# Kernel tuning notes

Measured on AMD Instinct MI355X. Metric: run time of the kernel, lower is better.

The kernel has to match this reference:

```python
import jax, jax.numpy as jnp
import numpy as np

B, L, D, NHEAD, NLAYERS = 2, 2048, 256, 8, 8
NAMES = ['self', 'cross'] * 4


def setup_inputs() -> dict:
    key = jax.random.key(0)
    ks = jax.random.split(key, 6)
    w_scale = D ** -0.5  # keep activations well-scaled
    return {
        'f0': jax.random.normal(ks[0], (B, L, D), dtype=jnp.float32),
        'f1': jax.random.normal(ks[1], (B, L, D), dtype=jnp.float32),
        'Wq': jax.random.normal(ks[2], (NLAYERS, D, D), dtype=jnp.float32) * w_scale,
        'Wk': jax.random.normal(ks[3], (NLAYERS, D, D), dtype=jnp.float32) * w_scale,
        'Wv': jax.random.normal(ks[4], (NLAYERS, D, D), dtype=jnp.float32) * w_scale,
        'Wo': jax.random.normal(ks[5], (NLAYERS, D, D), dtype=jnp.float32) * w_scale,
    }


def _rope(x, inv_freq):
    # x: (B, L, D); RoPE over the FULL model dim (matches original, mixes heads)
    L_, D_ = x.shape[1], x.shape[2]
    t = jnp.arange(L_, dtype=jnp.float32)
    freqs = t[:, None] * inv_freq[None, :]          # (L, D/2)
    emb = jnp.concatenate([freqs, freqs], axis=-1)  # (L, D)
    x1, x2 = x[..., : D_ // 2], x[..., D_ // 2:]
    rot = jnp.concatenate([-x2, x1], axis=-1)
    return x * jnp.cos(emb) + rot * jnp.sin(emb)


def _attn(x, src, wq, wk, wv, wo, use_rope, inv_freq):
    b, l1, d = x.shape
    l2 = src.shape[1]
    dh = d // NHEAD
    q = x @ wq.T    # torch Linear: x @ W^T
    k = src @ wk.T
    v = src @ wv.T
    if use_rope:
        q = _rope(q, inv_freq)
        k = _rope(k, inv_freq)
    q = q.reshape(b, l1, NHEAD, dh)
    k = k.reshape(b, l2, NHEAD, dh)
    v = v.reshape(b, l2, NHEAD, dh)
    scores = jnp.einsum('bqhd,bkhd->bhqk', q, k) * (dh ** -0.5)
    out = jnp.einsum('bhqk,bkhd->bqhd', jax.nn.softmax(scores, axis=-1), v)
    return out.reshape(b, l1, d) @ wo.T


def reference(f0, f1, Wq, Wk, Wv, Wo):
    d = f0.shape[-1]
    inv_freq = 1.0 / (10000.0 ** (jnp.arange(0, d, 2, dtype=jnp.float32) / d))
    for i, name in enumerate(NAMES):
        if name == 'self':
            f0 = f0 + _attn(f0, f0, Wq[i], Wk[i], Wv[i], Wo[i], True, inv_freq)
            f1 = f1 + _attn(f1, f1, Wq[i], Wk[i], Wv[i], Wo[i], True, inv_freq)
        else:
            # sequential updates: second cross uses the UPDATED f0 (matches torch)
            f0 = f0 + _attn(f0, f1, Wq[i], Wk[i], Wv[i], Wo[i], False, inv_freq)
            f1 = f1 + _attn(f1, f0, Wq[i], Wk[i], Wv[i], Wo[i], False, inv_freq)
    return (f0, f1)
```

## Files before the change

### kernel.cpp

```cpp
#include <hip/hip_runtime.h>

#define BB   2
#define LL   2048
#define DD   256
#define NH   8
#define MM   (BB*LL)
#define NLAYERS 8
#define MMDD ((size_t)MM*DD)

typedef unsigned short ushort_t;
typedef __attribute__((ext_vector_type(8))) short  short8;
typedef __attribute__((ext_vector_type(4))) float  f32x4;
typedef __attribute__((ext_vector_type(4))) unsigned int u32x4;
typedef __attribute__((ext_vector_type(2))) unsigned int u32x2;

#define CSC 0.2550500394f

#define WAITV2 asm volatile("s_waitcnt vmcnt(2)" ::: "memory")
#define WAITV0 asm volatile("s_waitcnt vmcnt(0)" ::: "memory")
#define WAITLG asm volatile("s_waitcnt lgkmcnt(0)" ::: "memory")
#define BAR()  __builtin_amdgcn_s_barrier()
#define SCHED0 __builtin_amdgcn_sched_barrier(0)

__device__ __forceinline__ f32x4 mfma16(short8 a, short8 b, f32x4 c) {
    return __builtin_amdgcn_mfma_f32_16x16x32_bf16(a, b, c, 0, 0, 0);
}
__device__ __forceinline__ unsigned cvtpk(float lo, float hi) {
    unsigned r;
    asm volatile("v_cvt_pk_bf16_f32 %0, %1, %2" : "=v"(r) : "v"(lo), "v"(hi));
    return r;
}
__device__ __forceinline__ void pl32(unsigned &a, unsigned &b) {
    asm volatile("v_permlane32_swap_b32 %0, %1" : "+v"(a), "+v"(b));
}
__device__ __forceinline__ float bf2f(unsigned short h) {
    return __builtin_bit_cast(float, ((unsigned)h) << 16);
}
__device__ __forceinline__ void gll16(const void* gsrc, void* ldst) {
    __builtin_amdgcn_global_load_lds(
        (const __attribute__((address_space(1))) unsigned int*)gsrc,
        (__attribute__((address_space(3))) unsigned int*)ldst, 16, 0, 0);
}


__global__ __launch_bounds__(256) void initf(const float* __restrict__ f0,
                                             const float* __restrict__ f1,
                                             float* __restrict__ F,
                                             ushort_t* __restrict__ Fb) {
    int i = blockIdx.x * 256 + threadIdx.x;
    const float* src = (i < 131072) ? f0 : f1;
    int loc = i & 131071;
    const f32x4* p = (const f32x4*)(src + (size_t)loc * 8);
    f32x4 a = p[0], b = p[1];
    *(f32x4*)&F[(size_t)i * 8]     = a;
    *(f32x4*)&F[(size_t)i * 8 + 4] = b;
    u32x4 o = {cvtpk(a.x, a.y), cvtpk(a.z, a.w), cvtpk(b.x, b.y), cvtpk(b.z, b.w)};
    *(u32x4*)&Fb[(size_t)i * 8] = o;
}

__global__ __launch_bounds__(256) void wconv(const float* __restrict__ a,
                                             const float* __restrict__ b,
                                             const float* __restrict__ c,
                                             const float* __restrict__ d,
                                             ushort_t* __restrict__ out) {
    int i = blockIdx.x * 256 + threadIdx.x;
    int reg = i >> 16, loc = i & 65535;
    const float* src = reg == 0 ? a : reg == 1 ? b : reg == 2 ? c : d;
    const f32x4* p = (const f32x4*)(src + (size_t)loc * 8);
    f32x4 x = p[0], y = p[1];
    u32x4 o = {cvtpk(x.x, x.y), cvtpk(x.z, x.w), cvtpk(y.x, y.y), cvtpk(y.z, y.w)};
    *(u32x4*)&out[(size_t)reg * 524288 + (size_t)loc * 8] = o;
}

__global__ __launch_bounds__(128) void rtab(float* __restrict__ tab) {
    int p = blockIdx.x, j = threadIdx.x;
    float inv = __expf(-((float)j / 128.f) * 9.210340371976184f);
    float s, c;
    sincosf((float)p * inv, &s, &c);
    tab[(size_t)p * 256 + j]       = c;
    tab[(size_t)p * 256 + 128 + j] = s;
}

__global__ __launch_bounds__(256) void rope_qk(ushort_t* __restrict__ Qio,
                                               const ushort_t* __restrict__ KSrc,
                                               ushort_t* __restrict__ KT,
                                               const float* __restrict__ tab) {
    const bool isq = (blockIdx.y == 0);
    const ushort_t* S = isq ? Qio : KSrc;
    int t = threadIdx.x;
    int row = blockIdx.x * 8 + (t >> 5);
    int jj = (t & 31) * 4;
    int pos = row & (LL - 1);
    u32x2 va = *(const u32x2*)&S[(size_t)row * 256 + jj];
    u32x2 vb = *(const u32x2*)&S[(size_t)row * 256 + 128 + jj];
    f32x4 a = {bf2f(va.x & 0xffff), bf2f(va.x >> 16),
               bf2f(va.y & 0xffff), bf2f(va.y >> 16)};
    f32x4 b = {bf2f(vb.x & 0xffff), bf2f(vb.x >> 16),
               bf2f(vb.y & 0xffff), bf2f(vb.y >> 16)};
    f32x4 c = *(const f32x4*)&tab[(size_t)pos * 256 + jj];
    f32x4 s = *(const f32x4*)&tab[(size_t)pos * 256 + 128 + jj];
    f32x4 o1 = a * c - b * s;
    f32x4 o2 = b * c + a * s;
    if (isq) { o1 *= CSC; o2 *= CSC; }
    u32x2 p1 = {cvtpk(o1.x, o1.y), cvtpk(o1.z, o1.w)};
    u32x2 p2 = {cvtpk(o2.x, o2.y), cvtpk(o2.z, o2.w)};
    if (isq) {
        *(u32x2*)&Qio[(size_t)row * 256 + jj]       = p1;
        *(u32x2*)&Qio[(size_t)row * 256 + 128 + jj] = p2;
    } else {
        int z = row >> 11, key = row & 2047;
        int tt = key >> 6, kk = key & 63;
        int hA = jj >> 5, dh = jj & 31;
        int g = dh >> 3, e = dh & 7;
        size_t base = (size_t)tt * 2048 + (size_t)g * 512 + (size_t)kk * 8 + e;
        *(u32x2*)&KT[(size_t)(z * 8 + hA) * 65536 + base]     = p1;
        *(u32x2*)&KT[(size_t)(z * 8 + hA + 4) * 65536 + base] = p2;
    }
}

template<int NQ, int NK, int NV, int QMODE, int KMODE, int NTY>
__global__ __launch_bounds__(256) void gemm5(const ushort_t* __restrict__ X,
                                             const ushort_t* __restrict__ WQ,
                                             const ushort_t* __restrict__ WK,
                                             const ushort_t* __restrict__ WV,
                                             ushort_t* __restrict__ DQ,
                                             ushort_t* __restrict__ DK,
                                             ushort_t* __restrict__ DVT) {
    constexpr int NTX = NQ + NK + NV;
    __shared__ ushort_t Xb[3][4096];
    __shared__ ushort_t Wb[3][4096];
    const int tid = threadIdx.x, ln = tid & 63, w = tid >> 6;
    const int f = blockIdx.x;
    const int xcd = f & 7, s = f >> 3;
    const int bx = s % NTX, byg = s / NTX;
    const int by = xcd * (NTY / 8) + byg;
    const int m0 = by * 64;

    const ushort_t* W; ushort_t* DH; int n0, mode;
    if (NQ && bx < NQ)           { W = WQ; DH = DQ;  mode = QMODE; n0 = bx * 64; }
    else if (NK && bx < NQ + NK) { W = WK; DH = DK;  mode = KMODE; n0 = (bx - NQ) * 64; }
    else                         { W = WV; DH = DVT; mode = 3; n0 = (bx - NQ - NK) * 64; }

    auto stage = [&](int c, int buf) {
#pragma unroll
        for (int i = 0; i < 2; i++) {
            int sl = (w * 2 + i) * 64 + ln;
            int r = sl >> 3, x = sl & 7;
            int col = c * 64 + ((x ^ (r & 7)) << 3);
            gll16(X + (size_t)(m0 + r) * 256 + col, &Xb[buf][(w * 2 + i) * 512]);
            gll16(W + (size_t)(n0 + r) * 256 + col, &Wb[buf][(w * 2 + i) * 512]);
        }
    };

    const int ql = ln & 15, gq = ln >> 4;
    const int wm = w >> 1, wn = w & 1;
    f32x4 z4 = {0.f, 0.f, 0.f, 0.f};
    f32x4 acc[2][2] = {{z4, z4}, {z4, z4}};

    stage(0, 0);
    stage(1, 1);
#pragma unroll
    for (int c = 0; c < 4; c++) {
        if (c < 3) { asm volatile("s_waitcnt vmcnt(4)" ::: "memory"); } else { WAITV0; }
        BAR(); SCHED0;
        if (c + 2 < 4) stage(c + 2, (c + 2) % 3);
        const ushort_t* XL = Xb[c % 3];
        const ushort_t* WL = Wb[c % 3];
        __builtin_amdgcn_s_setprio(1);
#pragma unroll
        for (int ks = 0; ks < 2; ks++) {
            int cc = ks * 4 + gq;
            int r0 = 32 * wm + ql, r1 = r0 + 16;
            int nr0 = 32 * wn + ql, nr1 = nr0 + 16;
            short8 a0 = *(const short8*)&XL[(r0 * 8 + (cc ^ (r0 & 7))) * 8];
            short8 a1 = *(const short8*)&XL[(r1 * 8 + (cc ^ (r1 & 7))) * 8];
            short8 b0 = *(const short8*)&WL[(nr0 * 8 + (cc ^ (nr0 & 7))) * 8];
            short8 b1 = *(const short8*)&WL[(nr1 * 8 + (cc ^ (nr1 & 7))) * 8];
            acc[0][0] = mfma16(a0, b0, acc[0][0]);
            acc[0][1] = mfma16(a0, b1, acc[0][1]);
            acc[1][0] = mfma16(a1, b0, acc[1][0]);
            acc[1][1] = mfma16(a1, b1, acc[1][1]);
        }
        __builtin_amdgcn_s_setprio(0);
    }

    if (mode == 3) {
        float* scr = (float*)&Xb[0][0];
        __syncthreads();
#pragma unroll
        for (int mf = 0; mf < 2; mf++)
#pragma unroll
            for (int nf = 0; nf < 2; nf++)
#pragma unroll
                for (int r = 0; r < 4; r++) {
                    int nloc = 32 * wn + 16 * nf + ql;
                    int mloc = 32 * wm + 16 * mf + 4 * gq + r;
                    scr[nloc * 65 + mloc] = acc[mf][nf][r];
                }
        __syncthreads();
        int nloc = tid >> 2, mc = (tid & 3) * 16;
        int ng = n0 + nloc, hh = ng >> 5, dh = ng & 31;
        int mg = m0 + mc;
        int z = mg >> 11, key = mg & 2047;
        int tt = key >> 6;
        int ks = (mc >> 5) & 1, J = (mc >> 4) & 1;
        int cA = 4 * ks + 2 * J, cB = cA + 1;
        int swz = dh & 7;
        const float* sc = &scr[nloc * 65 + mc];
        u32x2 q0 = {cvtpk(sc[0], sc[1]),   cvtpk(sc[2], sc[3])};
        u32x2 q1 = {cvtpk(sc[4], sc[5]),   cvtpk(sc[6], sc[7])};
        u32x2 q2 = {cvtpk(sc[8], sc[9]),   cvtpk(sc[10], sc[11])};
        u32x2 q3 = {cvtpk(sc[12], sc[13]), cvtpk(sc[14], sc[15])};
        ushort_t* base = &DVT[(size_t)(z * 8 + hh) * 65536 + (size_t)tt * 2048 + dh * 64];
        *(u32x2*)&base[(cA ^ swz) * 8]     = q0;
        *(u32x2*)&base[(cB ^ swz) * 8]     = q1;
        *(u32x2*)&base[(cA ^ swz) * 8 + 4] = q2;
        *(u32x2*)&base[(cB ^ swz) * 8 + 4] = q3;
    } else {
#pragma unroll
        for (int mf = 0; mf < 2; mf++)
#pragma unroll
            for (int nf = 0; nf < 2; nf++)
#pragma unroll
                for (int r = 0; r < 4; r++) {
                    int mg = m0 + 32 * wm + 16 * mf + gq * 4 + r;
                    int ng = n0 + 32 * wn + 16 * nf + ql;
                    float v = acc[mf][nf][r];
                    if (mode == 2) {
                        DH[(size_t)mg * 256 + ng] = (ushort_t)cvtpk(v, v);
                    } else if (mode == 5) {
                        int zh = (mg >> 11) * 8 + (ng >> 5);
                        size_t off = (size_t)zh * 65536
                                   + (size_t)((mg & 2047) >> 6) * 2048
                                   + (size_t)((ng & 31) >> 3) * 512
                                   + (size_t)(mg & 63) * 8 + (ng & 7);
                        DH[off] = (ushort_t)cvtpk(v, v);
                    } else {
                        float vs = v * CSC;
                        DH[(size_t)mg * 256 + ng] = (ushort_t)cvtpk(vs, vs);
                    }
                }
    }
}

template<int SPLIT, int NTY>
__global__ __launch_bounds__(256) void gemmO(const float* __restrict__ Op,
                                             const float* __restrict__ Lp,
                                             const ushort_t* __restrict__ W,
                                             const float* __restrict__ Res,
                                             float* __restrict__ OutF,
                                             ushort_t* __restrict__ OutH,
                                             int mrows) {
    __shared__ ushort_t Xf[64 * 256];
    __shared__ ushort_t Wpb[3][4096];
    const int tid = threadIdx.x, ln = tid & 63, w = tid >> 6;
    const int f = blockIdx.x;
    const int xcd = f & 7, s = f >> 3;
    const int bx = s & 3, byg = s >> 2;
    const int by = xcd * (NTY / 8) + byg;
    const int m0 = by * 64, n0 = bx * 64;

    auto stageW = [&](int c, int buf) {
#pragma unroll
        for (int i = 0; i < 2; i++) {
            int sl = (w * 2 + i) * 64 + ln;
            int r = sl >> 3, x = sl & 7;
            int col = c * 64 + ((x ^ (r & 7)) << 3);
            gll16(W + (size_t)(n0 + r) * 256 + col, &Wpb[buf][(w * 2 + i) * 512]);
        }
    };
    stageW(0, 0);
    stageW(1, 1);

    const int xr = tid >> 2, q = tid & 3, hb = q >> 1;
    float inv[4];
#pragma unroll
    for (int hh = 0; hh < 4; hh++) {
        float l = 0.f;
#pragma unroll
        for (int sp = 0; sp < SPLIT; sp++)
            l += Lp[(size_t)sp * mrows * 8 + (size_t)(m0 + xr) * 8 + 2 * hh + hb];
        inv[hh] = 1.f / l;
    }
#pragma unroll
    for (int p = 0; p < 4; p++) {
        int col = q * 16 + 64 * p;
        f32x4 a0 = {0.f,0.f,0.f,0.f}, a1 = a0, a2 = a0, a3 = a0;
#pragma unroll
        for (int sp = 0; sp < SPLIT; sp++) {
            const float* src = &Op[(size_t)sp * mrows * 256 + (size_t)(m0 + xr) * 256 + col];
            a0 += *(const f32x4*)&src[0];
            a1 += *(const f32x4*)&src[4];
            a2 += *(const f32x4*)&src[8];
            a3 += *(const f32x4*)&src[12];
        }
        float iv = inv[p];
        a0 *= iv; a1 *= iv; a2 *= iv; a3 *= iv;
        u32x4 w0 = {cvtpk(a0.x, a0.y), cvtpk(a0.z, a0.w),
                    cvtpk(a1.x, a1.y), cvtpk(a1.z, a1.w)};
        u32x4 w1 = {cvtpk(a2.x, a2.y), cvtpk(a2.z, a2.w),
                    cvtpk(a3.x, a3.y), cvtpk(a3.z, a3.w)};
        int xc0 = q * 2;
        *(u32x4*)&Xf[xr * 256 + p * 64 + ((xc0)     ^ (xr & 7)) * 8] = w0;
        *(u32x4*)&Xf[xr * 256 + p * 64 + ((xc0 + 1) ^ (xr & 7)) * 8] = w1;
    }
    WAITLG;
    BAR(); SCHED0;

    const int ql = ln & 15, gq = ln >> 4;
    const int wm = w >> 1, wn = w & 1;
    f32x4 z4 = {0.f, 0.f, 0.f, 0.f};
    f32x4 acc[2][2] = {{z4, z4}, {z4, z4}};
#pragma unroll
    for (int c = 0; c < 4; c++) {
        if (c < 3) { WAITV2; } else { WAITV0; }
        BAR(); SCHED0;
        if (c + 2 < 4) stageW(c + 2, (c + 2) % 3);
        const ushort_t* WL = Wpb[c % 3];
        __builtin_amdgcn_s_setprio(1);
#pragma unroll
        for (int ks = 0; ks < 2; ks++) {
            int cc = ks * 4 + gq;
            int r0 = 32 * wm + ql, r1 = r0 + 16;
            int nr0 = 32 * wn + ql, nr1 = nr0 + 16;
            short8 a0 = *(const short8*)&Xf[r0 * 256 + c * 64 + (cc ^ (r0 & 7)) * 8];
            short8 a1 = *(const short8*)&Xf[r1 * 256 + c * 64 + (cc ^ (r1 & 7)) * 8];
            short8 b0 = *(const short8*)&WL[(nr0 * 8 + (cc ^ (nr0 & 7))) * 8];
            short8 b1 = *(const short8*)&WL[(nr1 * 8 + (cc ^ (nr1 & 7))) * 8];
            acc[0][0] = mfma16(a0, b0, acc[0][0]);
            acc[0][1] = mfma16(a0, b1, acc[0][1]);
            acc[1][0] = mfma16(a1, b0, acc[1][0]);
            acc[1][1] = mfma16(a1, b1, acc[1][1]);
        }
        __builtin_amdgcn_s_setprio(0);
    }

#pragma unroll
    for (int mf = 0; mf < 2; mf++)
#pragma unroll
        for (int nf = 0; nf < 2; nf++)
#pragma unroll
            for (int r = 0; r < 4; r++) {
                int mg = m0 + 32 * wm + 16 * mf + gq * 4 + r;
                int ng = n0 + 32 * wn + 16 * nf + ql;
                size_t idx = (size_t)mg * 256 + ng;
                float o = Res[idx] + acc[mf][nf][r];
                OutF[idx] = o;
                OutH[idx] = (ushort_t)cvtpk(o, o);
            }
}

template<int SPLIT>
__global__ __launch_bounds__(256) void attn8(const ushort_t* __restrict__ Q,
                                             const ushort_t* __restrict__ K,
                                             const ushort_t* __restrict__ Vt,
                                             float* __restrict__ Op,
                                             float* __restrict__ Lp, int mrows) {
    constexpr int KEYS = 2048 / SPLIT;
    constexpr int NT = KEYS / 64;
    __shared__ ushort_t K_lds[3][2048];
    __shared__ ushort_t V_lds[3][2048];

    const int tid = threadIdx.x, ln = tid & 63, w = tid >> 6;
    const int ql = ln & 15, gq = ln >> 4;
    const int f = blockIdx.x;
    const int xcd = f & 7, slot = f >> 3;
    const int qb = slot & 15, gg = slot >> 4;
    const int h = xcd;
    const int zz = gg / SPLIT, sp = gg % SPLIT;
    const int q0 = qb * 128 + w * 32;
    const size_t rb = (size_t)zz * 2048;
    const int zh = zz * 8 + h;

    short8 qfA = *(const short8*)&Q[(rb + q0 + ql) * 256 + h * 32 + gq * 8];
    short8 qfB = *(const short8*)&Q[(rb + q0 + 16 + ql) * 256 + h * 32 + gq * 8];

    const ushort_t* kt = K  + (size_t)zh * 65536 + (size_t)sp * NT * 2048 + tid * 8;
    const ushort_t* vt = Vt + (size_t)zh * 65536 + (size_t)sp * NT * 2048 + tid * 8;

    gll16(kt,        &K_lds[0][w * 512]);
    gll16(vt,        &V_lds[0][w * 512]);
    gll16(kt + 2048, &K_lds[1][w * 512]);
    gll16(vt + 2048, &V_lds[1][w * 512]);

    const short os = (short)0x3F80;
    const short8 ones = {os, os, os, os, os, os, os, os};
    f32x4 z4 = {0.f, 0.f, 0.f, 0.f};
    f32x4 o0A = z4, o1A = z4, o0B = z4, o1B = z4, laccA = z4, laccB = z4;

    int cur = 0, pre = 2;
    for (int t = 0; t < NT; t++) {
        if (t < NT - 1) { WAITV2; } else { WAITV0; }
        BAR(); SCHED0;
        if (t + 2 < NT) {
            gll16(kt + (size_t)(t + 2) * 2048, &K_lds[pre][w * 512]);
            gll16(vt + (size_t)(t + 2) * 2048, &V_lds[pre][w * 512]);
        }
        const ushort_t* KL = K_lds[cur];
        const ushort_t* VL = V_lds[cur];

        f32x4 stA[4], stB[4];
        __builtin_amdgcn_s_setprio(1);
#pragma unroll
        for (int j = 0; j < 4; j++) {
            short8 kf = *(const short8*)&KL[(gq * 64 + 16 * j + ql) * 8];
            stA[j] = mfma16(kf, qfA, z4);
            stB[j] = mfma16(kf, qfB, z4);
        }
        __builtin_amdgcn_s_setprio(0);
#pragma unroll
        for (int j = 0; j < 4; j++)
#pragma unroll
            for (int r = 0; r < 4; r++) {
                stA[j][r] = __builtin_amdgcn_exp2f(stA[j][r]);
                stB[j][r] = __builtin_amdgcn_exp2f(stB[j][r]);
            }
        unsigned aLo[4], aHi[4], bLo[4], bHi[4];
#pragma unroll
        for (int j = 0; j < 4; j++) {
            aLo[j] = cvtpk(stA[j][0], stA[j][1]);
            aHi[j] = cvtpk(stA[j][2], stA[j][3]);
            bLo[j] = cvtpk(stB[j][0], stB[j][1]);
            bHi[j] = cvtpk(stB[j][2], stB[j][3]);
        }
        pl32(aLo[0], aLo[1]); pl32(aHi[0], aHi[1]);
        pl32(aLo[2], aLo[3]); pl32(aHi[2], aHi[3]);
        pl32(bLo[0], bLo[1]); pl32(bHi[0], bHi[1]);
        pl32(bLo[2], bLo[3]); pl32(bHi[2], bHi[3]);
        u32x4 fA0 = {aLo[0], aHi[0], aLo[1], aHi[1]};
        u32x4 fA1 = {aLo[2], aHi[2], aLo[3], aHi[3]};
        u32x4 fB0 = {bLo[0], bHi[0], bLo[1], bHi[1]};
        u32x4 fB1 = {bLo[2], bHi[2], bLo[3], bHi[3]};
        short8 pfA0 = __builtin_bit_cast(short8, fA0);
        short8 pfA1 = __builtin_bit_cast(short8, fA1);
        short8 pfB0 = __builtin_bit_cast(short8, fB0);
        short8 pfB1 = __builtin_bit_cast(short8, fB1);

        __builtin_amdgcn_s_setprio(1);
#pragma unroll
        for (int ks = 0; ks < 2; ks++) {
            int sw = (4 * ks + gq) ^ (ql & 7);
            short8 vf0 = *(const short8*)&VL[(ql * 8 + sw) * 8];
            short8 vf1 = *(const short8*)&VL[((16 + ql) * 8 + sw) * 8];
            short8 pA = ks ? pfA1 : pfA0;
            short8 pB = ks ? pfB1 : pfB0;
            o0A = mfma16(vf0, pA, o0A);
            o1A = mfma16(vf1, pA, o1A);
            o0B = mfma16(vf0, pB, o0B);
            o1B = mfma16(vf1, pB, o1B);
            laccA = mfma16(ones, pA, laccA);
            laccB = mfma16(ones, pB, laccB);
        }
        __builtin_amdgcn_s_setprio(0);
        cur = (cur == 2) ? 0 : cur + 1;
        pre = (pre == 2) ? 0 : pre + 1;
    }

    size_t rowA = rb + q0 + ql, rowB = rowA + 16;
    float* obA = Op + (size_t)sp * mrows * 256 + rowA * 256 + h * 32;
    float* obB = Op + (size_t)sp * mrows * 256 + rowB * 256 + h * 32;
    *(f32x4*)&obA[gq * 4]      = o0A;
    *(f32x4*)&obA[16 + gq * 4] = o1A;
    *(f32x4*)&obB[gq * 4]      = o0B;
    *(f32x4*)&obB[16 + gq * 4] = o1B;
    if (gq == 0) {
        Lp[(size_t)sp * mrows * 8 + rowA * 8 + h] = laccA[0];
        Lp[(size_t)sp * mrows * 8 + rowB * 8 + h] = laccB[0];
    }
}

extern "C" void kernel_launch(void* const* d_in, const int* in_sizes, int n_in,
                              void* d_out, int out_size, void* d_ws, size_t ws_size,
                              hipStream_t stream) {
    const float* f0_in = (const float*)d_in[0];
    const float* f1_in = (const float*)d_in[1];
    const float* Wq = (const float*)d_in[2];
    const float* Wk = (const float*)d_in[3];
    const float* Wv = (const float*)d_in[4];
    const float* Wo = (const float*)d_in[5];

    float* F0 = (float*)d_out;
    float* F1 = F0 + MMDD;

    ushort_t* Fb  = (ushort_t*)d_ws;
    ushort_t* Qb  = Fb  + 2 * MMDD;
    ushort_t* Khb = Qb  + 2 * MMDD;
    ushort_t* Vhb = Khb + 2 * MMDD;
    ushort_t* Tbb = Vhb + 2 * MMDD;
    ushort_t* Wb  = Tbb + 2 * MMDD;
    float*    Opw = (float*)(Wb + 2 * MMDD);
    float*    Lpw = Opw + (size_t)4 * MMDD;
    float*    tab = Lpw + 262144;

    ushort_t* Wqb = Wb;
    ushort_t* Wkb = Wb + (size_t)NLAYERS * 65536;
    ushort_t* Wvb = Wb + (size_t)2 * NLAYERS * 65536;
    ushort_t* Wob = Wb + (size_t)3 * NLAYERS * 65536;

    initf<<<1024, 256, 0, stream>>>(f0_in, f1_in, F0, Fb);
    wconv<<<1024, 256, 0, stream>>>(Wq, Wk, Wv, Wo, Wb);
    rtab<<<LL, 128, 0, stream>>>(tab);

    for (int i = 0; i < NLAYERS; i++) {
        const ushort_t* wq = Wqb + (size_t)i * 65536;
        const ushort_t* wk = Wkb + (size_t)i * 65536;
        const ushort_t* wv = Wvb + (size_t)i * 65536;
        const ushort_t* wo = Wob + (size_t)i * 65536;

        if ((i & 1) == 0) {
            gemm5<4, 4, 4, 2, 2, 128><<<1536, 256, 0, stream>>>(
                Fb, wq, wk, wv, Qb, Tbb, Vhb);
            rope_qk<<<dim3(1024, 2), 256, 0, stream>>>(Qb, Tbb, Khb, tab);
            attn8<2><<<1024, 256, 0, stream>>>(Qb, Khb, Vhb, Opw, Lpw, MM * 2);
            gemmO<2, 128><<<512, 256, 0, stream>>>(Opw, Lpw, wo, F0, F0, Fb, MM * 2);
        } else {
            gemm5<4, 0, 0, 4, 0, 128><<<512, 256, 0, stream>>>(
                Fb, wq, nullptr, nullptr, Qb, nullptr, nullptr);
            for (int s = 0; s < 2; s++) {
                const ushort_t* sb = Fb + (size_t)(1 - s) * MMDD;
                float* xf = s ? F1 : F0;
                ushort_t* xbw = Fb + (size_t)s * MMDD;
                gemm5<0, 4, 4, 0, 5, 64><<<512, 256, 0, stream>>>(
                    sb, nullptr, wk, wv, nullptr, Khb, Vhb);
                attn8<4><<<1024, 256, 0, stream>>>(Qb + (size_t)s * MMDD,
                                                   Khb, Vhb, Opw, Lpw, MM);
                gemmO<4, 64><<<256, 256, 0, stream>>>(Opw, Lpw, wo, xf, xf, xbw, MM);
            }
        }
    }
}
```

Baseline: 570.0 us.

## Fuse RoPE into QK GEMM epilogue, merge setup kernels, double-buffer attention

Adds a gemmQK kernel that computes Q and K projections with paired low/high half columns, so RoPE is applied in registers in the epilogue. This removes the separate rope_qk pass and its intermediate buffer. V is now projected by its own gemm5 launch. The three setup kernels are merged into one launch, and the attention kernel is restructured to stage 128 keys per double-buffered step instead of 64-key triple buffering. Risks include scalar 2-byte scattered stores in the gemmQK epilogue and one extra GEMM launch per self layer.

```diff
diff --git a/kernel.cpp b/kernel.cpp
--- a/kernel.cpp
+++ b/kernel.cpp
@@ -16,8 +16,10 @@
 
 #define CSC 0.2550500394f
 
+#define WAITV0 asm volatile("s_waitcnt vmcnt(0)" ::: "memory")
 #define WAITV2 asm volatile("s_waitcnt vmcnt(2)" ::: "memory")
-#define WAITV0 asm volatile("s_waitcnt vmcnt(0)" ::: "memory")
+#define WAITV4 asm volatile("s_waitcnt vmcnt(4)" ::: "memory")
+#define WAITV6 asm volatile("s_waitcnt vmcnt(6)" ::: "memory")
 #define WAITLG asm volatile("s_waitcnt lgkmcnt(0)" ::: "memory")
 #define BAR()  __builtin_amdgcn_s_barrier()
 #define SCHED0 __builtin_amdgcn_sched_barrier(0)
@@ -43,79 +45,145 @@
 }
 
 
-__global__ __launch_bounds__(256) void initf(const float* __restrict__ f0,
+__global__ __launch_bounds__(256) void setup(const float* __restrict__ f0,
                                              const float* __restrict__ f1,
+                                             const float* __restrict__ Wq,
+                                             const float* __restrict__ Wk,
+                                             const float* __restrict__ Wv,
+                                             const float* __restrict__ Wo,
                                              float* __restrict__ F,
-                                             ushort_t* __restrict__ Fb) {
-    int i = blockIdx.x * 256 + threadIdx.x;
-    const float* src = (i < 131072) ? f0 : f1;
-    int loc = i & 131071;
-    const f32x4* p = (const f32x4*)(src + (size_t)loc * 8);
-    f32x4 a = p[0], b = p[1];
-    *(f32x4*)&F[(size_t)i * 8]     = a;
-    *(f32x4*)&F[(size_t)i * 8 + 4] = b;
-    u32x4 o = {cvtpk(a.x, a.y), cvtpk(a.z, a.w), cvtpk(b.x, b.y), cvtpk(b.z, b.w)};
-    *(u32x4*)&Fb[(size_t)i * 8] = o;
-}
-
-__global__ __launch_bounds__(256) void wconv(const float* __restrict__ a,
-                                             const float* __restrict__ b,
-                                             const float* __restrict__ c,
-                                             const float* __restrict__ d,
-                                             ushort_t* __restrict__ out) {
-    int i = blockIdx.x * 256 + threadIdx.x;
-    int reg = i >> 16, loc = i & 65535;
-    const float* src = reg == 0 ? a : reg == 1 ? b : reg == 2 ? c : d;
-    const f32x4* p = (const f32x4*)(src + (size_t)loc * 8);
-    f32x4 x = p[0], y = p[1];
-    u32x4 o = {cvtpk(x.x, x.y), cvtpk(x.z, x.w), cvtpk(y.x, y.y), cvtpk(y.z, y.w)};
-    *(u32x4*)&out[(size_t)reg * 524288 + (size_t)loc * 8] = o;
-}
-
-__global__ __launch_bounds__(128) void rtab(float* __restrict__ tab) {
-    int p = blockIdx.x, j = threadIdx.x;
-    float inv = __expf(-((float)j / 128.f) * 9.210340371976184f);
-    float s, c;
-    sincosf((float)p * inv, &s, &c);
-    tab[(size_t)p * 256 + j]       = c;
-    tab[(size_t)p * 256 + 128 + j] = s;
-}
-
-__global__ __launch_bounds__(256) void rope_qk(ushort_t* __restrict__ Qio,
-                                               const ushort_t* __restrict__ KSrc,
-                                               ushort_t* __restrict__ KT,
-                                               const float* __restrict__ tab) {
-    const bool isq = (blockIdx.y == 0);
-    const ushort_t* S = isq ? Qio : KSrc;
-    int t = threadIdx.x;
-    int row = blockIdx.x * 8 + (t >> 5);
-    int jj = (t & 31) * 4;
-    int pos = row & (LL - 1);
-    u32x2 va = *(const u32x2*)&S[(size_t)row * 256 + jj];
-    u32x2 vb = *(const u32x2*)&S[(size_t)row * 256 + 128 + jj];
-    f32x4 a = {bf2f(va.x & 0xffff), bf2f(va.x >> 16),
-               bf2f(va.y & 0xffff), bf2f(va.y >> 16)};
-    f32x4 b = {bf2f(vb.x & 0xffff), bf2f(vb.x >> 16),
-               bf2f(vb.y & 0xffff), bf2f(vb.y >> 16)};
-    f32x4 c = *(const f32x4*)&tab[(size_t)pos * 256 + jj];
-    f32x4 s = *(const f32x4*)&tab[(size_t)pos * 256 + 128 + jj];
-    f32x4 o1 = a * c - b * s;
-    f32x4 o2 = b * c + a * s;
-    if (isq) { o1 *= CSC; o2 *= CSC; }
-    u32x2 p1 = {cvtpk(o1.x, o1.y), cvtpk(o1.z, o1.w)};
-    u32x2 p2 = {cvtpk(o2.x, o2.y), cvtpk(o2.z, o2.w)};
-    if (isq) {
-        *(u32x2*)&Qio[(size_t)row * 256 + jj]       = p1;
-        *(u32x2*)&Qio[(size_t)row * 256 + 128 + jj] = p2;
+                                             ushort_t* __restrict__ Fb,
+                                             ushort_t* __restrict__ Wb,
+                                             float* __restrict__ tab) {
+    int b = blockIdx.x, t = threadIdx.x;
+    if (b < 1024) {
+        int i = b * 256 + t;
+        const float* src = (i < 131072) ? f0 : f1;
+        int loc = i & 131071;
+        const f32x4* p = (const f32x4*)(src + (size_t)loc * 8);
+        f32x4 a = p[0], bb = p[1];
+        *(f32x4*)&F[(size_t)i * 8]     = a;
+        *(f32x4*)&F[(size_t)i * 8 + 4] = bb;
+        u32x4 o = {cvtpk(a.x, a.y), cvtpk(a.z, a.w), cvtpk(bb.x, bb.y), cvtpk(bb.z, bb.w)};
+        *(u32x4*)&Fb[(size_t)i * 8] = o;
+    } else if (b < 2048) {
+        int i = (b - 1024) * 256 + t;
+        int reg = i >> 16, loc = i & 65535;
+        const float* src = reg == 0 ? Wq : reg == 1 ? Wk : reg == 2 ? Wv : Wo;
+        const f32x4* p = (const f32x4*)(src + (size_t)loc * 8);
+        f32x4 x = p[0], y = p[1];
+        u32x4 o = {cvtpk(x.x, x.y), cvtpk(x.z, x.w), cvtpk(y.x, y.y), cvtpk(y.z, y.w)};
+        *(u32x4*)&Wb[(size_t)reg * 524288 + (size_t)loc * 8] = o;
     } else {
-        int z = row >> 11, key = row & 2047;
-        int tt = key >> 6, kk = key & 63;
-        int hA = jj >> 5, dh = jj & 31;
-        int g = dh >> 3, e = dh & 7;
-        size_t base = (size_t)tt * 2048 + (size_t)g * 512 + (size_t)kk * 8 + e;
-        *(u32x2*)&KT[(size_t)(z * 8 + hA) * 65536 + base]     = p1;
-        *(u32x2*)&KT[(size_t)(z * 8 + hA + 4) * 65536 + base] = p2;
-    }
+        int idx = (b - 2048) * 256 + t;
+        int p = idx >> 7, j = idx & 127;
+        float inv = __expf(-((float)j / 128.f) * 9.210340371976184f);
+        float s, c;
+        sincosf((float)p * inv, &s, &c);
+        tab[(size_t)p * 256 + j]       = c;
+        tab[(size_t)p * 256 + 128 + j] = s;
+    }
+}
+
+__global__ __launch_bounds__(256) void gemmQK(const ushort_t* __restrict__ X,
+                                              const ushort_t* __restrict__ WQ,
+                                              const ushort_t* __restrict__ WK,
+                                              ushort_t* __restrict__ DQ,
+                                              ushort_t* __restrict__ KT,
+                                              const float* __restrict__ tab) {
+    __shared__ ushort_t Xb[2][4096];
+    __shared__ ushort_t WbL[2][4096];
+    __shared__ ushort_t WbH[2][4096];
+    const int tid = threadIdx.x, ln = tid & 63, w = tid >> 6;
+    const int f = blockIdx.x;
+    const int xcd = f & 7, u = f >> 3;
+    const int bx = u & 3, byg = u >> 2;
+    const int mat = bx >> 1, cg = bx & 1;
+    const int by = xcd * 16 + byg;
+    const int m0 = by * 64, n0 = cg * 64;
+    const ushort_t* W = mat ? WK : WQ;
+
+    auto stage = [&](int c, int buf) {
+#pragma unroll
+        for (int i = 0; i < 2; i++) {
+            int sl = (w * 2 + i) * 64 + ln;
+            int r = sl >> 3, x = sl & 7;
+            int col = c * 64 + ((x ^ (r & 7)) << 3);
+            gll16(X + (size_t)(m0 + r) * 256 + col,       &Xb[buf][(w * 2 + i) * 512]);
+            gll16(W + (size_t)(n0 + r) * 256 + col,       &WbL[buf][(w * 2 + i) * 512]);
+            gll16(W + (size_t)(n0 + 128 + r) * 256 + col, &WbH[buf][(w * 2 + i) * 512]);
+        }
+    };
+
+    const int ql = ln & 15, gq = ln >> 4;
+    const int wm = w >> 1, wn = w & 1;
+    f32x4 z4 = {0.f, 0.f, 0.f, 0.f};
+    f32x4 accL[2][2] = {{z4, z4}, {z4, z4}};
+    f32x4 accH[2][2] = {{z4, z4}, {z4, z4}};
+
+    stage(0, 0);
+    stage(1, 1);
+#pragma unroll
+    for (int c = 0; c < 4; c++) {
+        if (c < 3) { WAITV6; } else { WAITV0; }
+        BAR(); SCHED0;
+        const ushort_t* XL = Xb[c & 1];
+        const ushort_t* WL = WbL[c & 1];
+        const ushort_t* WH = WbH[c & 1];
+        __builtin_amdgcn_s_setprio(1);
+#pragma unroll
+        for (int ks = 0; ks < 2; ks++) {
+            int cc = ks * 4 + gq;
+            int r0 = 32 * wm + ql, r1 = r0 + 16;
+            int nr0 = 32 * wn + ql, nr1 = nr0 + 16;
+            short8 a0 = *(const short8*)&XL[(r0 * 8 + (cc ^ (r0 & 7))) * 8];
+            short8 a1 = *(const short8*)&XL[(r1 * 8 + (cc ^ (r1 & 7))) * 8];
+            short8 l0 = *(const short8*)&WL[(nr0 * 8 + (cc ^ (nr0 & 7))) * 8];
+            short8 l1 = *(const short8*)&WL[(nr1 * 8 + (cc ^ (nr1 & 7))) * 8];
+            short8 h0 = *(const short8*)&WH[(nr0 * 8 + (cc ^ (nr0 & 7))) * 8];
+            short8 h1 = *(const short8*)&WH[(nr1 * 8 + (cc ^ (nr1 & 7))) * 8];
+            accL[0][0] = mfma16(a0, l0, accL[0][0]);
+            accL[0][1] = mfma16(a0, l1, accL[0][1]);
+            accL[1][0] = mfma16(a1, l0, accL[1][0]);
+            accL[1][1] = mfma16(a1, l1, accL[1][1]);
+            accH[0][0] = mfma16(a0, h0, accH[0][0]);
+            accH[0][1] = mfma16(a0, h1, accH[0][1]);
+            accH[1][0] = mfma16(a1, h0, accH[1][0]);
+            accH[1][1] = mfma16(a1, h1, accH[1][1]);
+        }
+        __builtin_amdgcn_s_setprio(0);
+        BAR();
+        if (c + 2 < 4) stage(c + 2, c & 1);
+    }
+
+#pragma unroll
+    for (int mf = 0; mf < 2; mf++)
+#pragma unroll
+        for (int nf = 0; nf < 2; nf++)
+#pragma unroll
+            for (int r = 0; r < 4; r++) {
+                int mg = m0 + 32 * wm + 16 * mf + gq * 4 + r;
+                int jl = n0 + 32 * wn + 16 * nf + ql;
+                int pos = mg & (LL - 1);
+                float a = accL[mf][nf][r], b = accH[mf][nf][r];
+                float c = tab[(size_t)pos * 256 + jl];
+                float s = tab[(size_t)pos * 256 + 128 + jl];
+                float o1 = a * c - b * s;
+                float o2 = b * c + a * s;
+                if (mat == 0) {
+                    o1 *= CSC; o2 *= CSC;
+                    DQ[(size_t)mg * 256 + jl]       = (ushort_t)cvtpk(o1, o1);
+                    DQ[(size_t)mg * 256 + jl + 128] = (ushort_t)cvtpk(o2, o2);
+                } else {
+                    int z = mg >> 11, key = mg & 2047;
+                    int tt = key >> 6, kk = key & 63;
+                    int dh = jl & 31, hA = jl >> 5;
+                    size_t base = (size_t)tt * 2048 + (size_t)(dh >> 3) * 512
+                                + (size_t)kk * 8 + (dh & 7);
+                    KT[(size_t)(z * 8 + hA) * 65536 + base]     = (ushort_t)cvtpk(o1, o1);
+                    KT[(size_t)(z * 8 + hA + 4) * 65536 + base] = (ushort_t)cvtpk(o2, o2);
+                }
+            }
 }
 
 template<int NQ, int NK, int NV, int QMODE, int KMODE, int NTY>
@@ -161,7 +229,7 @@
     stage(1, 1);
 #pragma unroll
     for (int c = 0; c < 4; c++) {
-        if (c < 3) { asm volatile("s_waitcnt vmcnt(4)" ::: "memory"); } else { WAITV0; }
+        if (c < 3) { WAITV4; } else { WAITV0; }
         BAR(); SCHED0;
         if (c + 2 < 4) stage(c + 2, (c + 2) % 3);
         const ushort_t* XL = Xb[c % 3];
@@ -351,15 +419,15 @@
 }
 
 template<int SPLIT>
-__global__ __launch_bounds__(256) void attn8(const ushort_t* __restrict__ Q,
+__global__ __launch_bounds__(256) void attn9(const ushort_t* __restrict__ Q,
                                              const ushort_t* __restrict__ K,
                                              const ushort_t* __restrict__ Vt,
                                              float* __restrict__ Op,
                                              float* __restrict__ Lp, int mrows) {
     constexpr int KEYS = 2048 / SPLIT;
-    constexpr int NT = KEYS / 64;
-    __shared__ ushort_t K_lds[3][2048];
-    __shared__ ushort_t V_lds[3][2048];
+    constexpr int NP = KEYS / 128;
+    __shared__ ushort_t K_lds[2][4096];
+    __shared__ ushort_t V_lds[2][4096];
 
     const int tid = threadIdx.x, ln = tid & 63, w = tid >> 6;
     const int ql = ln & 15, gq = ln >> 4;
@@ -375,85 +443,93 @@
     short8 qfA = *(const short8*)&Q[(rb + q0 + ql) * 256 + h * 32 + gq * 8];
     short8 qfB = *(const short8*)&Q[(rb + q0 + 16 + ql) * 256 + h * 32 + gq * 8];
 
-    const ushort_t* kt = K  + (size_t)zh * 65536 + (size_t)sp * NT * 2048 + tid * 8;
-    const ushort_t* vt = Vt + (size_t)zh * 65536 + (size_t)sp * NT * 2048 + tid * 8;
-
-    gll16(kt,        &K_lds[0][w * 512]);
-    gll16(vt,        &V_lds[0][w * 512]);
-    gll16(kt + 2048, &K_lds[1][w * 512]);
-    gll16(vt + 2048, &V_lds[1][w * 512]);
+    const ushort_t* kt = K  + (size_t)zh * 65536 + (size_t)sp * (KEYS / 64) * 2048
+                            + w * 1024 + ln * 8;
+    const ushort_t* vt = Vt + (size_t)zh * 65536 + (size_t)sp * (KEYS / 64) * 2048
+                            + w * 1024 + ln * 8;
+
+    auto stage = [&](int p, int buf) {
+        gll16(kt + (size_t)p * 4096,       &K_lds[buf][w * 1024]);
+        gll16(kt + (size_t)p * 4096 + 512, &K_lds[buf][w * 1024 + 512]);
+        gll16(vt + (size_t)p * 4096,       &V_lds[buf][w * 1024]);
+        gll16(vt + (size_t)p * 4096 + 512, &V_lds[buf][w * 1024 + 512]);
+    };
+    stage(0, 0);
+    stage(1, 1);
 
     const short os = (short)0x3F80;
     const short8 ones = {os, os, os, os, os, os, os, os};
     f32x4 z4 = {0.f, 0.f, 0.f, 0.f};
     f32x4 o0A = z4, o1A = z4, o0B = z4, o1B = z4, laccA = z4, laccB = z4;
 
-    int cur = 0, pre = 2;
-    for (int t = 0; t < NT; t++) {
-        if (t < NT - 1) { WAITV2; } else { WAITV0; }
+    for (int p = 0; p < NP; p++) {
+        if (p < NP - 1) { WAITV4; } else { WAITV0; }
         BAR(); SCHED0;
-        if (t + 2 < NT) {
-            gll16(kt + (size_t)(t + 2) * 2048, &K_lds[pre][w * 512]);
-            gll16(vt + (size_t)(t + 2) * 2048, &V_lds[pre][w * 512]);
-        }
-        const ushort_t* KL = K_lds[cur];
-        const ushort_t* VL = V_lds[cur];
-
-        f32x4 stA[4], stB[4];
+        const ushort_t* KL = K_lds[p & 1];
+        const ushort_t* VL = V_lds[p & 1];
+
+        short8 pA[4], pB[4];
+#pragma unroll
+        for (int h2 = 0; h2 < 2; h2++) {
+            const ushort_t* KLh = KL + h2 * 2048;
+            f32x4 sA[4], sB[4];
+            __builtin_amdgcn_s_setprio(1);
+#pragma unroll
+            for (int jj = 0; jj < 4; jj++) {
+                short8 kf = *(const short8*)&KLh[(gq * 64 + 16 * jj + ql) * 8];
+                sA[jj] = mfma16(kf, qfA, z4);
+                sB[jj] = mfma16(kf, qfB, z4);
+            }
+            __builtin_amdgcn_s_setprio(0);
+#pragma unroll
+            for (int jj = 0; jj < 4; jj++)
+#pragma unroll
+                for (int r = 0; r < 4; r++) {
+                    sA[jj][r] = __builtin_amdgcn_exp2f(sA[jj][r]);
+                    sB[jj][r] = __builtin_amdgcn_exp2f(sB[jj][r]);
+                }
+            unsigned aLo[4], aHi[4], bLo[4], bHi[4];
+#pragma unroll
+            for (int jj = 0; jj < 4; jj++) {
+                aLo[jj] = cvtpk(sA[jj][0], sA[jj][1]);
+                aHi[jj] = cvtpk(sA[jj][2], sA[jj][3]);
+                bLo[jj] = cvtpk(sB[jj][0], sB[jj][1]);
+                bHi[jj] = cvtpk(sB[jj][2], sB[jj][3]);
+            }
+            pl32(aLo[0], aLo[1]); pl32(aHi[0], aHi[1]);
+            pl32(aLo[2], aLo[3]); pl32(aHi[2], aHi[3]);
+            pl32(bLo[0], bLo[1]); pl32(bHi[0], bHi[1]);
+            pl32(bLo[2], bLo[3]); pl32(bHi[2], bHi[3]);
+            u32x4 fA0 = {aLo[0], aHi[0], aLo[1], aHi[1]};
+            u32x4 fA1 = {aLo[2], aHi[2], aLo[3], aHi[3]};
+            u32x4 fB0 = {bLo[0], bHi[0], bLo[1], bHi[1]};
+            u32x4 fB1 = {bLo[2], bHi[2], bLo[3], bHi[3]};
+            pA[h2 * 2]     = __builtin_bit_cast(short8, fA0);
+            pA[h2 * 2 + 1] = __builtin_bit_cast(short8, fA1);
+            pB[h2 * 2]     = __builtin_bit_cast(short8, fB0);
+            pB[h2 * 2 + 1] = __builtin_bit_cast(short8, fB1);
+        }
+
         __builtin_amdgcn_s_setprio(1);
 #pragma unroll
-        for (int j = 0; j < 4; j++) {
-            short8 kf = *(const short8*)&KL[(gq * 64 + 16 * j + ql) * 8];
-            stA[j] = mfma16(kf, qfA, z4);
-            stB[j] = mfma16(kf, qfB, z4);
+        for (int ks = 0; ks < 4; ks++) {
+            int img = ks >> 1, ks2 = ks & 1;
+            int sw = (4 * ks2 + gq) ^ (ql & 7);
+            short8 vf0 = *(const short8*)&VL[img * 2048 + (ql * 8 + sw) * 8];
+            short8 vf1 = *(const short8*)&VL[img * 2048 + ((16 + ql) * 8 + sw) * 8];
+            o0A = mfma16(vf0, pA[ks], o0A);
+            o1A = mfma16(vf1, pA[ks], o1A);
+            o0B = mfma16(vf0, pB[ks], o0B);
+            o1B = mfma16(vf1, pB[ks], o1B);
+            laccA = mfma16(ones, pA[ks], laccA);
+            laccB = mfma16(ones, pB[ks], laccB);
         }
         __builtin_amdgcn_s_setprio(0);
-#pragma unroll
-        for (int j = 0; j < 4; j++)
-#pragma unroll
-            for (int r = 0; r < 4; r++) {
-                stA[j][r] = __builtin_amdgcn_exp2f(stA[j][r]);
-                stB[j][r] = __builtin_amdgcn_exp2f(stB[j][r]);
-            }
-        unsigned aLo[4], aHi[4], bLo[4], bHi[4];
-#pragma unroll
-        for (int j = 0; j < 4; j++) {
-            aLo[j] = cvtpk(stA[j][0], stA[j][1]);
-            aHi[j] = cvtpk(stA[j][2], stA[j][3]);
-            bLo[j] = cvtpk(stB[j][0], stB[j][1]);
-            bHi[j] = cvtpk(stB[j][2], stB[j][3]);
-        }
-        pl32(aLo[0], aLo[1]); pl32(aHi[0], aHi[1]);
-        pl32(aLo[2], aLo[3]); pl32(aHi[2], aHi[3]);
-        pl32(bLo[0], bLo[1]); pl32(bHi[0], bHi[1]);
-        pl32(bLo[2], bLo[3]); pl32(bHi[2], bHi[3]);
-        u32x4 fA0 = {aLo[0], aHi[0], aLo[1], aHi[1]};
-        u32x4 fA1 = {aLo[2], aHi[2], aLo[3], aHi[3]};
-        u32x4 fB0 = {bLo[0], bHi[0], bLo[1], bHi[1]};
-        u32x4 fB1 = {bLo[2], bHi[2], bLo[3], bHi[3]};
-        short8 pfA0 = __builtin_bit_cast(short8, fA0);
-        short8 pfA1 = __builtin_bit_cast(short8, fA1);
-        short8 pfB0 = __builtin_bit_cast(short8, fB0);
-        short8 pfB1 = __builtin_bit_cast(short8, fB1);
-
-        __builtin_amdgcn_s_setprio(1);
-#pragma unroll
-        for (int ks = 0; ks < 2; ks++) {
-            int sw = (4 * ks + gq) ^ (ql & 7);
-            short8 vf0 = *(const short8*)&VL[(ql * 8 + sw) * 8];
-            short8 vf1 = *(const short8*)&VL[((16 + ql) * 8 + sw) * 8];
-            short8 pA = ks ? pfA1 : pfA0;
-            short8 pB = ks ? pfB1 : pfB0;
-            o0A = mfma16(vf0, pA, o0A);
-            o1A = mfma16(vf1, pA, o1A);
-            o0B = mfma16(vf0, pB, o0B);
-            o1B = mfma16(vf1, pB, o1B);
-            laccA = mfma16(ones, pA, laccA);
-            laccB = mfma16(ones, pB, laccB);
-        }
-        __builtin_amdgcn_s_setprio(0);
-        cur = (cur == 2) ? 0 : cur + 1;
-        pre = (pre == 2) ? 0 : pre + 1;
+
+        if (p + 2 < NP) {
+            BAR();
+            stage(p + 2, p & 1);
+        }
     }
 
     size_t rowA = rb + q0 + ql, rowB = rowA + 16;
@@ -486,8 +562,7 @@
     ushort_t* Qb  = Fb  + 2 * MMDD;
     ushort_t* Khb = Qb  + 2 * MMDD;
     ushort_t* Vhb = Khb + 2 * MMDD;
-    ushort_t* Tbb = Vhb + 2 * MMDD;
-    ushort_t* Wb  = Tbb + 2 * MMDD;
+    ushort_t* Wb  = Vhb + 2 * MMDD;
     float*    Opw = (float*)(Wb + 2 * MMDD);
     float*    Lpw = Opw + (size_t)4 * MMDD;
     float*    tab = Lpw + 262144;
@@ -497,9 +572,7 @@
     ushort_t* Wvb = Wb + (size_t)2 * NLAYERS * 65536;
     ushort_t* Wob = Wb + (size_t)3 * NLAYERS * 65536;
 
-    initf<<<1024, 256, 0, stream>>>(f0_in, f1_in, F0, Fb);
-    wconv<<<1024, 256, 0, stream>>>(Wq, Wk, Wv, Wo, Wb);
-    rtab<<<LL, 128, 0, stream>>>(tab);
+    setup<<<3072, 256, 0, stream>>>(f0_in, f1_in, Wq, Wk, Wv, Wo, F0, Fb, Wb, tab);
 
     for (int i = 0; i < NLAYERS; i++) {
         const ushort_t* wq = Wqb + (size_t)i * 65536;
@@ -508,10 +581,10 @@
         const ushort_t* wo = Wob + (size_t)i * 65536;
 
         if ((i & 1) == 0) {
-            gemm5<4, 4, 4, 2, 2, 128><<<1536, 256, 0, stream>>>(
-                Fb, wq, wk, wv, Qb, Tbb, Vhb);
-            rope_qk<<<dim3(1024, 2), 256, 0, stream>>>(Qb, Tbb, Khb, tab);
-            attn8<2><<<1024, 256, 0, stream>>>(Qb, Khb, Vhb, Opw, Lpw, MM * 2);
+            gemmQK<<<512, 256, 0, stream>>>(Fb, wq, wk, Qb, Khb, tab);
+            gemm5<0, 0, 4, 0, 0, 128><<<512, 256, 0, stream>>>(
+                Fb, nullptr, nullptr, wv, nullptr, nullptr, Vhb);
+            attn9<2><<<1024, 256, 0, stream>>>(Qb, Khb, Vhb, Opw, Lpw, MM * 2);
             gemmO<2, 128><<<512, 256, 0, stream>>>(Opw, Lpw, wo, F0, F0, Fb, MM * 2);
         } else {
             gemm5<4, 0, 0, 4, 0, 128><<<512, 256, 0, stream>>>(
@@ -522,7 +595,7 @@
                 ushort_t* xbw = Fb + (size_t)s * MMDD;
                 gemm5<0, 4, 4, 0, 5, 64><<<512, 256, 0, stream>>>(
                     sb, nullptr, wk, wv, nullptr, Khb, Vhb);
-                attn8<4><<<1024, 256, 0, stream>>>(Qb + (size_t)s * MMDD,
+                attn9<4><<<1024, 256, 0, stream>>>(Qb + (size_t)s * MMDD,
                                                    Khb, Vhb, Opw, Lpw, MM);
                 gemmO<4, 64><<<256, 256, 0, stream>>>(Opw, Lpw, wo, xf, xf, xbw, MM);
             }
```

New measurement: 560.0 us. About the same (-1.8%).
